# Optimization experiments

Measured on AMD Instinct MI355X. Metric: run time of the kernel, lower is better.

The kernel has to match this reference:

```python
import jax, jax.numpy as jnp
import numpy as np

N_NODES = 50000
HIDDEN = 128

def _gcn_conv(x, src, dst, W, b, n_nodes):
    # PyG GCNConv: out = D^{-1/2} (A+I) D^{-1/2} X W + b, self-loops already in src/dst
    h = x @ W                                   # [N, D]
    ones = jnp.ones(dst.shape[0], dtype=x.dtype)
    deg = jax.ops.segment_sum(ones, dst, num_segments=n_nodes)  # in-degree incl self-loop
    dinv = jnp.where(deg > 0, jax.lax.rsqrt(deg), 0.0)
    norm = dinv[src] * dinv[dst]                # [E]
    msgs = h[src] * norm[:, None]               # gather + scale, [E, D]
    out = jax.ops.segment_sum(msgs, dst, num_segments=n_nodes)  # scatter-add
    return out + b

def _layernorm(h, gamma, beta, eps=1e-5):
    mu = jnp.mean(h, axis=-1, keepdims=True)
    var = jnp.mean(jnp.square(h - mu), axis=-1, keepdims=True)
    return (h - mu) * jax.lax.rsqrt(var + eps) * gamma + beta

def setup_inputs() -> dict:
    key = jax.random.key(0)
    ks = jax.random.split(key, 8)
    x = jax.random.normal(ks[0], (N_NODES, HIDDEN), dtype=jnp.float32)
    edge_index = jax.random.randint(ks[1], (2, 600000), 0, N_NODES, dtype=jnp.int64)
    s = 1.0 / np.sqrt(HIDDEN)
    W1 = jax.random.uniform(ks[2], (HIDDEN, HIDDEN), jnp.float32, -s, s)
    b1 = jnp.zeros((HIDDEN,), jnp.float32)
    W2 = jax.random.uniform(ks[3], (HIDDEN, HIDDEN), jnp.float32, -s, s)
    b2 = jnp.zeros((HIDDEN,), jnp.float32)
    g1 = jnp.ones((HIDDEN,), jnp.float32); be1 = jnp.zeros((HIDDEN,), jnp.float32)
    g2 = jnp.ones((HIDDEN,), jnp.float32); be2 = jnp.zeros((HIDDEN,), jnp.float32)
    return {"x": x, "edge_index": edge_index, "W1": W1, "b1": b1, "W2": W2, "b2": b2,
            "g1": g1, "be1": be1, "g2": g2, "be2": be2}

def reference(x, edge_index, W1, b1, W2, b2, g1, be1, g2, be2):
    n = x.shape[0]
    loops = jnp.arange(n, dtype=edge_index.dtype)
    src = jnp.concatenate([edge_index[0], loops])   # add self-loops (PyG default)
    dst = jnp.concatenate([edge_index[1], loops])
    h = _gcn_conv(x, src, dst, W1, b1, n)
    h = jax.nn.gelu(_layernorm(h, g1, be1), approximate=False)
    h = _gcn_conv(h, src, dst, W2, b2, n)
    h = jax.nn.gelu(_layernorm(h, g2, be2), approximate=False)
    return h
```

## Files before the change

### kernel.cpp

```cpp
#include <hip/hip_runtime.h>
#include <math.h>

#define N_NODES 50000
#define HID 128
#define N_EDGES 600000
#define SEG_CAP 64

typedef __attribute__((ext_vector_type(8))) short s16x8;
typedef __attribute__((ext_vector_type(4))) float f32x4;
typedef __attribute__((ext_vector_type(4))) uint u32x4;

__device__ __forceinline__ ushort f2b(float f) {
    uint x = __builtin_bit_cast(uint, f);
    uint r = (x + 0x7FFFu + ((x >> 16) & 1u)) >> 16;
    return (ushort)r;
}
__device__ __forceinline__ float blo(uint u) {
    return __builtin_bit_cast(float, u << 16);
}
__device__ __forceinline__ float bhi(uint u) {
    return __builtin_bit_cast(float, u & 0xffff0000u);
}
__device__ __forceinline__ float gelu_exact(float y) {
    return 0.5f * y * (1.0f + erff(y * 0.70710678118654752f));
}

__global__ __launch_bounds__(256) void prep_kernel(
        const float* __restrict__ W1, const float* __restrict__ W2,
        uint* __restrict__ wfrag, u32x4* __restrict__ cnt4, int n4,
        u32x4* __restrict__ hs4) {
    int id = blockIdx.x * 256 + threadIdx.x;
    if (id < 16384) {
        const float* W = (id < 8192) ? W1 : W2;
        int q = id & 8191;
        int l16 = q & 15;
        int w   = (q >> 4) & 3;
        int kg  = (q >> 6) & 3;
        int f   = q >> 8;
        int n  = (f >> 2) * 16 + l16;
        int k0 = (f & 3) * 32 + kg * 8 + 2 * w;
        uint lo = f2b(W[(size_t)k0 * HID + n]);
        uint hi = f2b(W[(size_t)(k0 + 1) * HID + n]);
        size_t widx = ((size_t)(id >> 13) * 8192) +
                      ((size_t)f * 64 + kg * 16 + l16) * 4 + w;
        wfrag[widx] = lo | (hi << 16);
    } else if (id < 16384 + n4) {
        cnt4[id - 16384] = (u32x4)(0u);
    } else if (id < 16384 + n4 + 16) {
        hs4[(size_t)N_NODES * 16 + (id - 16384 - n4)] = (u32x4)(0u);
    }
}

__global__ void fill_fixed_kernel(const int4* __restrict__ src4,
                                  const int4* __restrict__ dst4,
                                  int* __restrict__ cnt,
                                  int* __restrict__ srcPerm, int e4) {
    int i = blockIdx.x * blockDim.x + threadIdx.x;
    if (i < e4) {
        int4 s = src4[i];
        int4 d = dst4[i];
        int p;
        p = atomicAdd(&cnt[d.x], 1); if (p < SEG_CAP) srcPerm[(d.x << 6) + p] = s.x;
        p = atomicAdd(&cnt[d.y], 1); if (p < SEG_CAP) srcPerm[(d.y << 6) + p] = s.y;
        p = atomicAdd(&cnt[d.z], 1); if (p < SEG_CAP) srcPerm[(d.z << 6) + p] = s.z;
        p = atomicAdd(&cnt[d.w], 1); if (p < SEG_CAP) srcPerm[(d.w << 6) + p] = s.w;
    }
}

template<bool AB16>
__device__ __forceinline__ void gemm_body(
        int bid, const void* __restrict__ Ap, const uint* __restrict__ wfrag,
        const int* __restrict__ cnt, uint* __restrict__ H, int M) {
    __shared__ u32x4 Wl[2048];
    const u32x4* wf4 = (const u32x4*)wfrag;
#pragma unroll
    for (int i = 0; i < 4; ++i)
        Wl[threadIdx.x + i * 512] = wf4[threadIdx.x + i * 512];
    __syncthreads();

    const int l  = threadIdx.x & 63;
    const int wv = threadIdx.x >> 6;
    const int r0 = bid * 128 + wv * 16;
    if (r0 >= M) return;
    const int arow = r0 + (l & 15);
    const int kg = l >> 4;
    const int l16 = l & 15;

    s16x8 afr[4];
    if (AB16) {
        const ushort* A = (const ushort*)Ap + (size_t)arow * HID;
#pragma unroll
        for (int ks = 0; ks < 4; ++ks)
            afr[ks] = __builtin_nontemporal_load(
                          (const s16x8*)(A + ks * 32 + kg * 8));
    } else {
        const float* A = (const float*)Ap + (size_t)arow * HID;
#pragma unroll
        for (int ks = 0; ks < 4; ++ks) {
            int k0 = ks * 32 + kg * 8;
            f32x4 a0 = __builtin_nontemporal_load((const f32x4*)(A + k0));
            f32x4 a1 = __builtin_nontemporal_load((const f32x4*)(A + k0 + 4));
            s16x8 v;
            v[0] = (short)f2b(a0.x); v[1] = (short)f2b(a0.y);
            v[2] = (short)f2b(a0.z); v[3] = (short)f2b(a0.w);
            v[4] = (short)f2b(a1.x); v[5] = (short)f2b(a1.y);
            v[6] = (short)f2b(a1.z); v[7] = (short)f2b(a1.w);
            afr[ks] = v;
        }
    }

    float drv[4];
#pragma unroll
    for (int q = 0; q < 4; ++q)
        drv[q] = rsqrtf((float)(cnt[r0 + kg * 4 + q] + 1));

    f32x4 acc[8];
#pragma unroll
    for (int ct = 0; ct < 8; ++ct) acc[ct] = (f32x4)(0.f);

    const ushort* Wls = (const ushort*)Wl;
#pragma unroll
    for (int ct = 0; ct < 8; ++ct) {
#pragma unroll
        for (int ks = 0; ks < 4; ++ks) {
            s16x8 bfr = *(const s16x8*)(Wls + ((ct * 4 + ks) * 64 + l) * 8);
            acc[ct] = __builtin_amdgcn_mfma_f32_16x16x32_bf16(
                          afr[ks], bfr, acc[ct], 0, 0, 0);
        }
    }

#pragma unroll
    for (int s = 0; s < 4; ++s) {
#pragma unroll
        for (int q = 0; q < 4; ++q) {
            int row = r0 + kg * 4 + q;
            uint wlo = f2b(acc[2 * s][q] * drv[q]);
            uint whi = f2b(acc[2 * s + 1][q] * drv[q]);
            H[(size_t)row * 64 + s * 16 + l16] = wlo | (whi << 16);
        }
    }
}

__global__ __launch_bounds__(512) void gemm1_kernel(
        const float* __restrict__ x, const uint* __restrict__ wfrag,
        const int* __restrict__ cnt, uint* __restrict__ H) {
    gemm_body<false>(blockIdx.x, x, wfrag, cnt, H, N_NODES);
}

__global__ __launch_bounds__(512) void gemm2_kernel(
        const ushort* __restrict__ z1, const uint* __restrict__ wfrag,
        const int* __restrict__ cnt, uint* __restrict__ H) {
    gemm_body<true>(blockIdx.x, z1, wfrag, cnt, H, N_NODES);
}

template<bool OUT_F32>
__global__ __launch_bounds__(256) void agg_ln_kernel(
        const u32x4* __restrict__ hs4, const int* __restrict__ cnt,
        const int* __restrict__ srcPerm,
        const float* __restrict__ b, const float* __restrict__ g,
        const float* __restrict__ be,
        ushort* __restrict__ z1, float* __restrict__ outf) {
    const int tid = threadIdx.x;
    const int l   = tid & 63;
    const int wv  = tid >> 6;
    const int l16 = l & 15;
    const int sg  = l >> 4;
    const int d   = blockIdx.x * 4 + wv;
    const int colL = ((l16 >> 2) << 5) + ((l16 & 3) << 2);

    u32x4 u0 = hs4[(uint)(d * 16 + l16)];
    const int degRaw = cnt[d];
    const int deg = (degRaw < SEG_CAP) ? degRaw : SEG_CAP;

    float aL[4] = {0.f, 0.f, 0.f, 0.f};
    float aH[4] = {0.f, 0.f, 0.f, 0.f};

    int idx = (l < deg) ? srcPerm[(d << 6) + l] : N_NODES;
    const int nBatch = (deg + 15) >> 4;
    for (int bi = 0; bi < nBatch; ++bi) {
        u32x4 uu[4];
#pragma unroll
        for (int c = 0; c < 4; ++c) {
            int s = __shfl(idx, bi * 16 + c * 4 + sg);
            uu[c] = hs4[(uint)(s * 16 + l16)];
        }
#pragma unroll
        for (int c = 0; c < 4; ++c) {
#pragma unroll
            for (int k = 0; k < 4; ++k) {
                aL[k] += blo(uu[c][k]);
                aH[k] += bhi(uu[c][k]);
            }
        }
    }

#pragma unroll
    for (int k = 0; k < 4; ++k) {
        aL[k] += __shfl_xor(aL[k], 16); aL[k] += __shfl_xor(aL[k], 32);
        aH[k] += __shfl_xor(aH[k], 16); aH[k] += __shfl_xor(aH[k], 32);
        aL[k] += blo(u0[k]);
        aH[k] += bhi(u0[k]);
    }

    const float dd = rsqrtf((float)(degRaw + 1));
    f32x4 bL = *(const f32x4*)&b[colL];
    f32x4 bH = *(const f32x4*)&b[colL + 16];
    float vL[4], vH[4];
    float s = 0.f, s2 = 0.f;
#pragma unroll
    for (int k = 0; k < 4; ++k) {
        vL[k] = aL[k] * dd + bL[k];
        vH[k] = aH[k] * dd + bH[k];
        s  += vL[k] + vH[k];
        s2 += vL[k] * vL[k] + vH[k] * vH[k];
    }
#pragma unroll
    for (int off = 1; off < 16; off <<= 1) {
        s  += __shfl_xor(s,  off);
        s2 += __shfl_xor(s2, off);
    }
    float mu   = s  * (1.0f / 128.0f);
    float var  = s2 * (1.0f / 128.0f) - mu * mu;
    float rstd = rsqrtf(var + 1e-5f);

    int c0 = colL + sg, c1 = colL + 16 + sg;
    float o0 = gelu_exact((vL[sg] - mu) * rstd * g[c0] + be[c0]);
    float o1 = gelu_exact((vH[sg] - mu) * rstd * g[c1] + be[c1]);

    if (OUT_F32) {
        outf[(size_t)d * HID + c0] = o0;
        outf[(size_t)d * HID + c1] = o1;
    } else {
        z1[(size_t)d * HID + c0] = f2b(o0);
        z1[(size_t)d * HID + c1] = f2b(o1);
    }
}

extern "C" void kernel_launch(void* const* d_in, const int* in_sizes, int n_in,
                              void* d_out, int out_size, void* d_ws, size_t ws_size,
                              hipStream_t stream) {
    const float* x   = (const float*)d_in[0];
    const int*   ei  = (const int*)d_in[1];
    const float* W1  = (const float*)d_in[2];
    const float* b1  = (const float*)d_in[3];
    const float* W2  = (const float*)d_in[4];
    const float* b2  = (const float*)d_in[5];
    const float* g1  = (const float*)d_in[6];
    const float* be1 = (const float*)d_in[7];
    const float* g2  = (const float*)d_in[8];
    const float* be2 = (const float*)d_in[9];
    float* out = (float*)d_out;

    const int4* src4 = (const int4*)ei;
    const int4* dst4 = (const int4*)(ei + N_EDGES);

    uint*   hs      = (uint*)d_ws;
    ushort* z1      = (ushort*)(hs + (size_t)(N_NODES + 1) * 64);
    int*    srcPerm = (int*)(z1 + (size_t)N_NODES * HID);
    int*    cnt     = srcPerm + (size_t)N_NODES * SEG_CAP;
    uint*   wfrag   = (uint*)(cnt + 50016);

    const int B = 256;
    const int e4 = N_EDGES / 4;
    const int edge4B = (e4 + B - 1) / B;
    const int gemm_blocks = (N_NODES + 127) / 128;
    const int agg_blocks  = N_NODES / 4;
    const int zero4 = 50016 / 4;
    const int prepB = (16384 + zero4 + 16 + B - 1) / B;

    prep_kernel<<<prepB, B, 0, stream>>>(W1, W2, wfrag, (u32x4*)cnt, zero4,
                                         (u32x4*)hs);
    fill_fixed_kernel<<<edge4B, B, 0, stream>>>(src4, dst4, cnt, srcPerm, e4);

    gemm1_kernel<<<gemm_blocks, 512, 0, stream>>>(x, wfrag, cnt, hs);
    agg_ln_kernel<false><<<agg_blocks, B, 0, stream>>>(
        (const u32x4*)hs, cnt, srcPerm, b1, g1, be1, z1, nullptr);

    gemm2_kernel<<<gemm_blocks, 512, 0, stream>>>(z1, wfrag + 8192, cnt, hs);
    agg_ln_kernel<true><<<agg_blocks, B, 0, stream>>>(
        (const u32x4*)hs, cnt, srcPerm, b2, g2, be2, nullptr, out);
}
```

Before: 143.6 us.

## Fuse layer-1 aggregation/LayerNorm/GELU with layer-2 GEMM via shared memory

The first aggregation+LayerNorm+GELU and the second GEMM now run in one kernel. Each 512-thread block aggregates 16 nodes, stages the bf16 activations in shared memory, and runs the MFMA GEMM against W2 held in shared memory. Output goes to a second feature buffer, so the z1 round trip through global memory and one launch disappear. The cost is that each block reloads the whole 32 KB W2 fragment for only 16 rows. The block also does scattered 2-byte stores and has lower per-block parallelism in the GEMM stage.

```diff
diff --git a/kernel.cpp b/kernel.cpp
--- a/kernel.cpp
+++ b/kernel.cpp
@@ -28,7 +28,7 @@
 __global__ __launch_bounds__(256) void prep_kernel(
         const float* __restrict__ W1, const float* __restrict__ W2,
         uint* __restrict__ wfrag, u32x4* __restrict__ cnt4, int n4,
-        u32x4* __restrict__ hs4) {
+        u32x4* __restrict__ hsA4, u32x4* __restrict__ hsB4) {
     int id = blockIdx.x * 256 + threadIdx.x;
     if (id < 16384) {
         const float* W = (id < 8192) ? W1 : W2;
@@ -47,7 +47,9 @@
     } else if (id < 16384 + n4) {
         cnt4[id - 16384] = (u32x4)(0u);
     } else if (id < 16384 + n4 + 16) {
-        hs4[(size_t)N_NODES * 16 + (id - 16384 - n4)] = (u32x4)(0u);
+        hsA4[(size_t)N_NODES * 16 + (id - 16384 - n4)] = (u32x4)(0u);
+    } else if (id < 16384 + n4 + 32) {
+        hsB4[(size_t)N_NODES * 16 + (id - 16384 - n4 - 16)] = (u32x4)(0u);
     }
 }
 
@@ -67,10 +69,9 @@
     }
 }
 
-template<bool AB16>
-__device__ __forceinline__ void gemm_body(
-        int bid, const void* __restrict__ Ap, const uint* __restrict__ wfrag,
-        const int* __restrict__ cnt, uint* __restrict__ H, int M) {
+__global__ __launch_bounds__(512) void gemm1_kernel(
+        const float* __restrict__ x, const uint* __restrict__ wfrag,
+        const int* __restrict__ cnt, uint* __restrict__ H) {
     __shared__ u32x4 Wl[2048];
     const u32x4* wf4 = (const u32x4*)wfrag;
 #pragma unroll
@@ -80,33 +81,25 @@
 
     const int l  = threadIdx.x & 63;
     const int wv = threadIdx.x >> 6;
-    const int r0 = bid * 128 + wv * 16;
-    if (r0 >= M) return;
+    const int r0 = blockIdx.x * 128 + wv * 16;
+    if (r0 >= N_NODES) return;
     const int arow = r0 + (l & 15);
     const int kg = l >> 4;
     const int l16 = l & 15;
 
     s16x8 afr[4];
-    if (AB16) {
-        const ushort* A = (const ushort*)Ap + (size_t)arow * HID;
-#pragma unroll
-        for (int ks = 0; ks < 4; ++ks)
-            afr[ks] = __builtin_nontemporal_load(
-                          (const s16x8*)(A + ks * 32 + kg * 8));
-    } else {
-        const float* A = (const float*)Ap + (size_t)arow * HID;
-#pragma unroll
-        for (int ks = 0; ks < 4; ++ks) {
-            int k0 = ks * 32 + kg * 8;
-            f32x4 a0 = __builtin_nontemporal_load((const f32x4*)(A + k0));
-            f32x4 a1 = __builtin_nontemporal_load((const f32x4*)(A + k0 + 4));
-            s16x8 v;
-            v[0] = (short)f2b(a0.x); v[1] = (short)f2b(a0.y);
-            v[2] = (short)f2b(a0.z); v[3] = (short)f2b(a0.w);
-            v[4] = (short)f2b(a1.x); v[5] = (short)f2b(a1.y);
-            v[6] = (short)f2b(a1.z); v[7] = (short)f2b(a1.w);
-            afr[ks] = v;
-        }
+    const float* A = x + (size_t)arow * HID;
+#pragma unroll
+    for (int ks = 0; ks < 4; ++ks) {
+        int k0 = ks * 32 + kg * 8;
+        f32x4 a0 = __builtin_nontemporal_load((const f32x4*)(A + k0));
+        f32x4 a1 = __builtin_nontemporal_load((const f32x4*)(A + k0 + 4));
+        s16x8 v;
+        v[0] = (short)f2b(a0.x); v[1] = (short)f2b(a0.y);
+        v[2] = (short)f2b(a0.z); v[3] = (short)f2b(a0.w);
+        v[4] = (short)f2b(a1.x); v[5] = (short)f2b(a1.y);
+        v[6] = (short)f2b(a1.z); v[7] = (short)f2b(a1.w);
+        afr[ks] = v;
     }
 
     float drv[4];
@@ -141,25 +134,119 @@
     }
 }
 
-__global__ __launch_bounds__(512) void gemm1_kernel(
-        const float* __restrict__ x, const uint* __restrict__ wfrag,
-        const int* __restrict__ cnt, uint* __restrict__ H) {
-    gemm_body<false>(blockIdx.x, x, wfrag, cnt, H, N_NODES);
-}
-
-__global__ __launch_bounds__(512) void gemm2_kernel(
-        const ushort* __restrict__ z1, const uint* __restrict__ wfrag,
-        const int* __restrict__ cnt, uint* __restrict__ H) {
-    gemm_body<true>(blockIdx.x, z1, wfrag, cnt, H, N_NODES);
-}
-
-template<bool OUT_F32>
-__global__ __launch_bounds__(256) void agg_ln_kernel(
+__global__ __launch_bounds__(512) void agg1_gemm2_kernel(
+        const u32x4* __restrict__ hsA, const int* __restrict__ cnt,
+        const int* __restrict__ srcPerm,
+        const float* __restrict__ b, const float* __restrict__ g,
+        const float* __restrict__ be,
+        const uint* __restrict__ wfrag2, uint* __restrict__ hsB) {
+    __shared__ u32x4 Wl[2048];
+    __shared__ __attribute__((aligned(16))) ushort zt[16 * 136];
+    const int tid = threadIdx.x;
+    const u32x4* wf4 = (const u32x4*)wfrag2;
+#pragma unroll
+    for (int i = 0; i < 4; ++i)
+        Wl[tid + i * 512] = wf4[tid + i * 512];
+
+    const int l   = tid & 63;
+    const int wv  = tid >> 6;
+    const int l16 = l & 15;
+    const int sg  = l >> 4;
+    const int colL = ((l16 >> 2) << 5) + ((l16 & 3) << 2);
+
+    for (int t = 0; t < 2; ++t) {
+        const int nb = wv * 2 + t;
+        const int d  = blockIdx.x * 16 + nb;
+        u32x4 u0 = hsA[(uint)(d * 16 + l16)];
+        const int degRaw = cnt[d];
+        const int deg = (degRaw < SEG_CAP) ? degRaw : SEG_CAP;
+
+        float aL[4] = {0.f, 0.f, 0.f, 0.f};
+        float aH[4] = {0.f, 0.f, 0.f, 0.f};
+
+        int idx = (l < deg) ? srcPerm[(d << 6) + l] : N_NODES;
+        const int nBatch = (deg + 15) >> 4;
+        for (int bi = 0; bi < nBatch; ++bi) {
+            u32x4 uu[4];
+#pragma unroll
+            for (int c = 0; c < 4; ++c) {
+                int s = __shfl(idx, bi * 16 + c * 4 + sg);
+                uu[c] = hsA[(uint)(s * 16 + l16)];
+            }
+#pragma unroll
+            for (int c = 0; c < 4; ++c) {
+#pragma unroll
+                for (int k = 0; k < 4; ++k) {
+                    aL[k] += blo(uu[c][k]);
+                    aH[k] += bhi(uu[c][k]);
+                }
+            }
+        }
+#pragma unroll
+        for (int k = 0; k < 4; ++k) {
+            aL[k] += __shfl_xor(aL[k], 16); aL[k] += __shfl_xor(aL[k], 32);
+            aH[k] += __shfl_xor(aH[k], 16); aH[k] += __shfl_xor(aH[k], 32);
+            aL[k] += blo(u0[k]);
+            aH[k] += bhi(u0[k]);
+        }
+        const float dd = rsqrtf((float)(degRaw + 1));
+        f32x4 bL = *(const f32x4*)&b[colL];
+        f32x4 bH = *(const f32x4*)&b[colL + 16];
+        float vL[4], vH[4];
+        float s = 0.f, s2 = 0.f;
+#pragma unroll
+        for (int k = 0; k < 4; ++k) {
+            vL[k] = aL[k] * dd + bL[k];
+            vH[k] = aH[k] * dd + bH[k];
+            s  += vL[k] + vH[k];
+            s2 += vL[k] * vL[k] + vH[k] * vH[k];
+        }
+#pragma unroll
+        for (int off = 1; off < 16; off <<= 1) {
+            s  += __shfl_xor(s,  off);
+            s2 += __shfl_xor(s2, off);
+        }
+        float mu   = s  * (1.0f / 128.0f);
+        float var  = s2 * (1.0f / 128.0f) - mu * mu;
+        float rstd = rsqrtf(var + 1e-5f);
+        int c0 = colL + sg, c1 = colL + 16 + sg;
+        float o0 = gelu_exact((vL[sg] - mu) * rstd * g[c0] + be[c0]);
+        float o1 = gelu_exact((vH[sg] - mu) * rstd * g[c1] + be[c1]);
+        zt[nb * 136 + c0] = f2b(o0);
+        zt[nb * 136 + c1] = f2b(o1);
+    }
+    __syncthreads();
+
+    const int ct = wv;
+    const int kg = l >> 4;
+    s16x8 afr[4];
+#pragma unroll
+    for (int ks = 0; ks < 4; ++ks)
+        afr[ks] = *(const s16x8*)(zt + l16 * 136 + ks * 32 + kg * 8);
+
+    f32x4 acc = (f32x4)(0.f);
+    const ushort* Wls = (const ushort*)Wl;
+#pragma unroll
+    for (int ks = 0; ks < 4; ++ks) {
+        s16x8 bfr = *(const s16x8*)(Wls + ((ct * 4 + ks) * 64 + l) * 8);
+        acc = __builtin_amdgcn_mfma_f32_16x16x32_bf16(afr[ks], bfr, acc, 0, 0, 0);
+    }
+
+    const int sIdx = ct >> 1, hi = ct & 1;
+    ushort* H16 = (ushort*)hsB;
+#pragma unroll
+    for (int q = 0; q < 4; ++q) {
+        int row = blockIdx.x * 16 + kg * 4 + q;
+        float drv = rsqrtf((float)(cnt[row] + 1));
+        H16[(size_t)row * 128 + (sIdx * 16 + l16) * 2 + hi] = f2b(acc[q] * drv);
+    }
+}
+
+__global__ __launch_bounds__(256) void agg2_kernel(
         const u32x4* __restrict__ hs4, const int* __restrict__ cnt,
         const int* __restrict__ srcPerm,
         const float* __restrict__ b, const float* __restrict__ g,
-        const float* __restrict__ be,
-        ushort* __restrict__ z1, float* __restrict__ outf) {
+        const float* __restrict__ be, float* __restrict__ outf) {
     const int tid = threadIdx.x;
     const int l   = tid & 63;
     const int wv  = tid >> 6;
@@ -193,7 +280,6 @@
             }
         }
     }
-
 #pragma unroll
     for (int k = 0; k < 4; ++k) {
         aL[k] += __shfl_xor(aL[k], 16); aL[k] += __shfl_xor(aL[k], 32);
@@ -226,14 +312,8 @@
     int c0 = colL + sg, c1 = colL + 16 + sg;
     float o0 = gelu_exact((vL[sg] - mu) * rstd * g[c0] + be[c0]);
     float o1 = gelu_exact((vH[sg] - mu) * rstd * g[c1] + be[c1]);
-
-    if (OUT_F32) {
-        outf[(size_t)d * HID + c0] = o0;
-        outf[(size_t)d * HID + c1] = o1;
-    } else {
-        z1[(size_t)d * HID + c0] = f2b(o0);
-        z1[(size_t)d * HID + c1] = f2b(o1);
-    }
+    outf[(size_t)d * HID + c0] = o0;
+    outf[(size_t)d * HID + c1] = o1;
 }
 
 extern "C" void kernel_launch(void* const* d_in, const int* in_sizes, int n_in,
@@ -254,29 +334,28 @@
     const int4* src4 = (const int4*)ei;
     const int4* dst4 = (const int4*)(ei + N_EDGES);
 
-    uint*   hs      = (uint*)d_ws;
-    ushort* z1      = (ushort*)(hs + (size_t)(N_NODES + 1) * 64);
-    int*    srcPerm = (int*)(z1 + (size_t)N_NODES * HID);
-    int*    cnt     = srcPerm + (size_t)N_NODES * SEG_CAP;
-    uint*   wfrag   = (uint*)(cnt + 50016);
+    uint* hsA     = (uint*)d_ws;
+    uint* hsB     = hsA + (size_t)(N_NODES + 1) * 64;
+    int*  srcPerm = (int*)(hsB + (size_t)(N_NODES + 1) * 64);
+    int*  cnt     = srcPerm + (size_t)N_NODES * SEG_CAP;
+    uint* wfrag   = (uint*)(cnt + 50016);
 
     const int B = 256;
     const int e4 = N_EDGES / 4;
     const int edge4B = (e4 + B - 1) / B;
-    const int gemm_blocks = (N_NODES + 127) / 128;
-    const int agg_blocks  = N_NODES / 4;
+    const int gemm_blocks  = (N_NODES + 127) / 128;
+    const int fused_blocks = N_NODES / 16;
+    const int agg2_blocks  = N_NODES / 4;
     const int zero4 = 50016 / 4;
-    const int prepB = (16384 + zero4 + 16 + B - 1) / B;
+    const int prepB = (16384 + zero4 + 32 + B - 1) / B;
 
     prep_kernel<<<prepB, B, 0, stream>>>(W1, W2, wfrag, (u32x4*)cnt, zero4,
-                                         (u32x4*)hs);
+                                         (u32x4*)hsA, (u32x4*)hsB);
     fill_fixed_kernel<<<edge4B, B, 0, stream>>>(src4, dst4, cnt, srcPerm, e4);
 
-    gemm1_kernel<<<gemm_blocks, 512, 0, stream>>>(x, wfrag, cnt, hs);
-    agg_ln_kernel<false><<<agg_blocks, B, 0, stream>>>(
-        (const u32x4*)hs, cnt, srcPerm, b1, g1, be1, z1, nullptr);
-
-    gemm2_kernel<<<gemm_blocks, 512, 0, stream>>>(z1, wfrag + 8192, cnt, hs);
-    agg_ln_kernel<true><<<agg_blocks, B, 0, stream>>>(
-        (const u32x4*)hs, cnt, srcPerm, b2, g2, be2, nullptr, out);
-}
+    gemm1_kernel<<<gemm_blocks, 512, 0, stream>>>(x, wfrag, cnt, hsA);
+    agg1_gemm2_kernel<<<fused_blocks, 512, 0, stream>>>(
+        (const u32x4*)hsA, cnt, srcPerm, b1, g1, be1, wfrag + 8192, hsB);
+    agg2_kernel<<<agg2_blocks, B, 0, stream>>>(
+        (const u32x4*)hsB, cnt, srcPerm, b2, g2, be2, out);
+}
```

After: 131.3 us (median of 2 runs). 1.09x faster.
